# Optimization experiments

Hardware: AMD Instinct MI355X
Metric: run time of the kernel (lower is better)

The kernel has to match this reference:

```python
import jax, jax.numpy as jnp
import numpy as np

B, S, H = 128, 4096, 128

def setup_inputs() -> dict:
    key = jax.random.key(0)
    ks = jax.random.split(key, 6)
    return {
        "nodes_hidden": jax.random.normal(ks[0], (B, S, H), dtype=jnp.float32),
        "new_nodes": jax.random.normal(ks[1], (B, 1, H), dtype=jnp.float32),
        "W1": jax.random.normal(ks[2], (2 * H, 256), dtype=jnp.float32) * 0.06,
        "b1": jnp.zeros((256,), dtype=jnp.float32),
        "W2": jax.random.normal(ks[3], (256, 64), dtype=jnp.float32) * 0.06,
        "b2": jnp.zeros((64,), dtype=jnp.float32),
        "W3": jax.random.normal(ks[4], (64, 1), dtype=jnp.float32) * 0.1,
        "b3": jnp.zeros((1,), dtype=jnp.float32),
    }

def reference(nodes_hidden, new_nodes, W1, b1, W2, b2, W3, b3):
    # new_nodes: [B,1,H] -> broadcast over S; concat on feature axis -> [B,S,2H]
    new = jnp.broadcast_to(new_nodes, nodes_hidden.shape)
    con = jnp.concatenate([nodes_hidden, new], axis=-1)  # [B,S,2H]
    # MLP (dropout inactive at inference): 2H -> 256 -> 64 -> 1, batched over B*S
    h1 = jax.nn.relu(jnp.einsum('bsf,fk->bsk', con, W1) + b1)
    h2 = jax.nn.relu(jnp.einsum('bsk,km->bsm', h1, W2) + b2)
    out = jax.nn.sigmoid(jnp.einsum('bsm,mo->bso', h2, W3) + b3)  # [B,S,1]
    return jnp.squeeze(out, axis=-1)  # [B,S]
```

## Files before the change

kernel.cpp:

```cpp
#include <hip/hip_runtime.h>
#include <hip/hip_bf16.h>
#include <cstdint>
#include <cstddef>

#define BB 128
#define SS 4096
#define HH 128
#define N1 256
#define N2 64
#define BROWS 128

typedef __bf16 bf16x8 __attribute__((ext_vector_type(8)));
typedef __bf16 bf16x4 __attribute__((ext_vector_type(4)));
typedef float  f32x4  __attribute__((ext_vector_type(4)));

__global__ __launch_bounds__(256) void conv_weights(
    const float* __restrict__ W1, const float* __restrict__ W2,
    __bf16* __restrict__ w1f, __bf16* __restrict__ w2f)
{
    int tid = blockIdx.x * 256 + threadIdx.x;
    if (tid < 4096) {
        int lane = tid & 63, ks = (tid >> 6) & 3, g = tid >> 8;
        int col = 16 * g + (lane & 15);
        int kbase = 32 * ks + 8 * (lane >> 4);
        bf16x8 v;
#pragma unroll
        for (int j = 0; j < 8; ++j) v[j] = (__bf16)W1[(size_t)(kbase + j) * N1 + col];
        *(bf16x8*)(w1f + (size_t)tid * 8) = v;
    } else if (tid < 6144) {
        int s = tid - 4096;
        int lane = s & 63, ksp = (s >> 6) & 7, mt2 = s >> 9;
        int q = lane >> 4, ln = lane & 15;
        bf16x8 v;
#pragma unroll
        for (int j = 0; j < 8; ++j) {
            int c = 32 * ksp + 16 * (j >> 2) + 4 * q + (j & 3);
            v[j] = (__bf16)W2[(size_t)c * N2 + 16 * mt2 + ln];
        }
        *(bf16x8*)(w2f + (size_t)s * 8) = v;
    }
}

__global__ __launch_bounds__(256) void an_partial(
    const float* __restrict__ W1, const float* __restrict__ b1,
    const float* __restrict__ newn, __bf16* __restrict__ an)
{
    const int b = blockIdx.x, c = threadIdx.x;
    float acc = b1[c];
    const float* wp = W1 + (size_t)HH * N1 + c;
    const float* nv = newn + (size_t)b * HH;
#pragma unroll 8
    for (int k = 0; k < HH; ++k)
        acc = fmaf(nv[k], wp[(size_t)k * N1], acc);
    an[(size_t)b * N1 + c] = (__bf16)acc;
}

__global__ __launch_bounds__(256, 4) void edge_mlp_mfma4(
    const float* __restrict__ nodes,
    const float* __restrict__ b2,
    const float* __restrict__ W3, const float* __restrict__ b3,
    const __bf16* __restrict__ w1f, const __bf16* __restrict__ w2f,
    const __bf16* __restrict__ an,
    float* __restrict__ out)
{
    __shared__ __bf16 X[BROWS * HH];

    const int t = threadIdx.x;
    const int w = t >> 6, l = t & 63, q = l >> 4, ln = l & 15;
    const size_t row0 = (size_t)blockIdx.x * BROWS;
    const int b = (int)(row0 >> 12);

#pragma unroll
    for (int i = 0; i < 8; ++i) {
        int idx = i * 256 + t;
        int r = idx >> 4, c8 = idx & 15;
        const float* s = nodes + (row0 + r) * HH + 8 * c8;
        float4 f0 = *(const float4*)s, f1 = *(const float4*)(s + 4);
        bf16x8 v;
        v[0] = (__bf16)f0.x; v[1] = (__bf16)f0.y; v[2] = (__bf16)f0.z; v[3] = (__bf16)f0.w;
        v[4] = (__bf16)f1.x; v[5] = (__bf16)f1.y; v[6] = (__bf16)f1.z; v[7] = (__bf16)f1.w;
        int unit = c8 ^ (r & 7);
        *(bf16x8*)&X[(size_t)(r * 16 + unit) * 8] = v;
    }
    __syncthreads();

    f32x4 acc2[2][4];
#pragma unroll
    for (int mt2 = 0; mt2 < 4; ++mt2) {
        float4 bv = *(const float4*)(b2 + 16 * mt2 + 4 * q);
#pragma unroll
        for (int rs = 0; rs < 2; ++rs) {
            acc2[rs][mt2][0] = bv.x; acc2[rs][mt2][1] = bv.y;
            acc2[rs][mt2][2] = bv.z; acc2[rs][mt2][3] = bv.w;
        }
    }

    const __bf16* anb = an + (size_t)b * N1;

#pragma unroll 1
    for (int ksp = 0; ksp < 8; ++ksp) {
        bf16x8 af0[4], af1[4], a2f[4];
#pragma unroll
        for (int ks = 0; ks < 4; ++ks) {
            af0[ks] = *(const bf16x8*)(w1f + ((size_t)((2 * ksp)     * 4 + ks) * 64 + l) * 8);
            af1[ks] = *(const bf16x8*)(w1f + ((size_t)((2 * ksp + 1) * 4 + ks) * 64 + l) * 8);
        }
#pragma unroll
        for (int mt2 = 0; mt2 < 4; ++mt2)
            a2f[mt2] = *(const bf16x8*)(w2f + ((size_t)(mt2 * 8 + ksp) * 64 + l) * 8);

        f32x4 an0, an1;
        {
            bf16x4 a0 = *(const bf16x4*)(anb + 32 * ksp + 4 * q);
            bf16x4 a1 = *(const bf16x4*)(anb + 32 * ksp + 16 + 4 * q);
#pragma unroll
            for (int j = 0; j < 4; ++j) { an0[j] = (float)a0[j]; an1[j] = (float)a1[j]; }
        }

#pragma unroll
        for (int rs = 0; rs < 2; ++rs) {
            const int r = 32 * w + 16 * rs + ln;
            const int rx = ln & 7;
            f32x4 alo = an0, ahi = an1;
#pragma unroll
            for (int ks = 0; ks < 4; ++ks) {
                bf16x8 xv = *(const bf16x8*)&X[(size_t)(r * 16 + ((4 * ks + q) ^ rx)) * 8];
                alo = __builtin_amdgcn_mfma_f32_16x16x32_bf16(af0[ks], xv, alo, 0, 0, 0);
                ahi = __builtin_amdgcn_mfma_f32_16x16x32_bf16(af1[ks], xv, ahi, 0, 0, 0);
            }
            bf16x8 bfrag;
#pragma unroll
            for (int j = 0; j < 4; ++j) {
                bfrag[j]     = (__bf16)fmaxf(alo[j], 0.0f);
                bfrag[4 + j] = (__bf16)fmaxf(ahi[j], 0.0f);
            }
#pragma unroll
            for (int mt2 = 0; mt2 < 4; ++mt2)
                acc2[rs][mt2] = __builtin_amdgcn_mfma_f32_16x16x32_bf16(a2f[mt2], bfrag, acc2[rs][mt2], 0, 0, 0);
        }
    }

    const float b3v = b3[0];
#pragma unroll
    for (int rs = 0; rs < 2; ++rs) {
        float sum = 0.f;
#pragma unroll
        for (int mt2 = 0; mt2 < 4; ++mt2) {
            float4 w3v = *(const float4*)(W3 + 16 * mt2 + 4 * q);
            sum += fmaxf(acc2[rs][mt2][0], 0.f) * w3v.x
                 + fmaxf(acc2[rs][mt2][1], 0.f) * w3v.y
                 + fmaxf(acc2[rs][mt2][2], 0.f) * w3v.z
                 + fmaxf(acc2[rs][mt2][3], 0.f) * w3v.w;
        }
        sum += __shfl_xor(sum, 16, 64);
        sum += __shfl_xor(sum, 32, 64);
        if (q == 0) {
            float v = sum + b3v;
            out[row0 + 32 * w + 16 * rs + ln] = 1.0f / (1.0f + __expf(-v));
        }
    }
}

__global__ __launch_bounds__(256, 4) void edge_mlp_f32(
    const float* __restrict__ nodes, const float* __restrict__ newn,
    const float* __restrict__ W1, const float* __restrict__ b1,
    const float* __restrict__ W2, const float* __restrict__ b2,
    const float* __restrict__ W3, const float* __restrict__ b3,
    float* __restrict__ out)
{
    __shared__ float buf[32][256];
    const int t = threadIdx.x;
    const long r0 = (long)blockIdx.x * 32;
    const int b = (int)(r0 >> 12);
    const float4* src = (const float4*)(nodes + (size_t)r0 * HH);
#pragma unroll
    for (int i = 0; i < 4; ++i) {
        int idx = t + i * 256;
        *(float4*)&buf[idx >> 5][(idx & 31) * 4] = src[idx];
    }
    {
        float nv = newn[b * HH + (t & 127)];
        for (int r = (t >> 7); r < 32; r += 2) buf[r][HH + (t & 127)] = nv;
    }
    __syncthreads();
    const int c0 = t & 63, rb = (t >> 6) * 8;
    float acc[8][4];
#pragma unroll
    for (int ci = 0; ci < 4; ++ci) {
        float bv = b1[c0 + 64 * ci];
#pragma unroll
        for (int r = 0; r < 8; ++r) acc[r][ci] = bv;
    }
    for (int k = 0; k < 256; k += 4) {
        float wv[4][4];
#pragma unroll
        for (int kk = 0; kk < 4; ++kk)
#pragma unroll
            for (int ci = 0; ci < 4; ++ci) wv[kk][ci] = W1[(k + kk) * N1 + c0 + 64 * ci];
#pragma unroll
        for (int r = 0; r < 8; ++r) {
            float4 x = *(const float4*)&buf[rb + r][k];
#pragma unroll
            for (int ci = 0; ci < 4; ++ci) {
                acc[r][ci] = fmaf(x.x, wv[0][ci], acc[r][ci]);
                acc[r][ci] = fmaf(x.y, wv[1][ci], acc[r][ci]);
                acc[r][ci] = fmaf(x.z, wv[2][ci], acc[r][ci]);
                acc[r][ci] = fmaf(x.w, wv[3][ci], acc[r][ci]);
            }
        }
    }
    __syncthreads();
#pragma unroll
    for (int r = 0; r < 8; ++r)
#pragma unroll
        for (int ci = 0; ci < 4; ++ci) buf[rb + r][c0 + 64 * ci] = fmaxf(acc[r][ci], 0.0f);
    __syncthreads();
    const int c2 = t & 31, g2 = t >> 5;
    float acc2[4][2];
#pragma unroll
    for (int cj = 0; cj < 2; ++cj) {
        float bv = b2[c2 + 32 * cj];
#pragma unroll
        for (int rr = 0; rr < 4; ++rr) acc2[rr][cj] = bv;
    }
    for (int k = 0; k < 256; k += 4) {
        float w2v[4][2];
#pragma unroll
        for (int kk = 0; kk < 4; ++kk)
#pragma unroll
            for (int cj = 0; cj < 2; ++cj) w2v[kk][cj] = W2[(k + kk) * N2 + c2 + 32 * cj];
#pragma unroll
        for (int rr = 0; rr < 4; ++rr) {
            float4 x = *(const float4*)&buf[4 * g2 + rr][k];
#pragma unroll
            for (int cj = 0; cj < 2; ++cj) {
                acc2[rr][cj] = fmaf(x.x, w2v[0][cj], acc2[rr][cj]);
                acc2[rr][cj] = fmaf(x.y, w2v[1][cj], acc2[rr][cj]);
                acc2[rr][cj] = fmaf(x.z, w2v[2][cj], acc2[rr][cj]);
                acc2[rr][cj] = fmaf(x.w, w2v[3][cj], acc2[rr][cj]);
            }
        }
    }
    const float w3a = W3[c2], w3b = W3[c2 + 32], b3v = b3[0];
    float p[4];
#pragma unroll
    for (int rr = 0; rr < 4; ++rr)
        p[rr] = fmaf(fmaxf(acc2[rr][0], 0.f), w3a, fmaxf(acc2[rr][1], 0.f) * w3b);
#pragma unroll
    for (int off = 16; off >= 1; off >>= 1)
#pragma unroll
        for (int rr = 0; rr < 4; ++rr) p[rr] += __shfl_xor(p[rr], off, 64);
    if (c2 == 0)
#pragma unroll
        for (int rr = 0; rr < 4; ++rr)
            out[r0 + 4 * g2 + rr] = 1.0f / (1.0f + __expf(-(p[rr] + b3v)));
}

extern "C" void kernel_launch(void* const* d_in, const int* in_sizes, int n_in,
                              void* d_out, int out_size, void* d_ws, size_t ws_size,
                              hipStream_t stream) {
    const float* nodes = (const float*)d_in[0];
    const float* newn  = (const float*)d_in[1];
    const float* W1    = (const float*)d_in[2];
    const float* b1    = (const float*)d_in[3];
    const float* W2    = (const float*)d_in[4];
    const float* b2    = (const float*)d_in[5];
    const float* W3    = (const float*)d_in[6];
    const float* b3    = (const float*)d_in[7];
    float* out = (float*)d_out;
    const int M = BB * SS;

    if (ws_size >= 163840) {
        __bf16* w1f = (__bf16*)d_ws;
        __bf16* w2f = (__bf16*)d_ws + 32768;
        __bf16* anp = (__bf16*)d_ws + 49152;
        hipLaunchKernelGGL(conv_weights, dim3(24), dim3(256), 0, stream, W1, W2, w1f, w2f);
        hipLaunchKernelGGL(an_partial, dim3(BB), dim3(256), 0, stream, W1, b1, newn, anp);
        hipLaunchKernelGGL(edge_mlp_mfma4, dim3(M / BROWS), dim3(256), 0, stream,
                           nodes, b2, W3, b3, w1f, w2f, anp, out);
    } else {
        hipLaunchKernelGGL(edge_mlp_f32, dim3(M / 32), dim3(256), 0, stream,
                           nodes, newn, W1, b1, W2, b2, W3, b3, out);
    }
}
```

Baseline: 97.76 us.

## Load node rows directly into MFMA fragments, drop LDS staging, double rows per block

Result: no change. 96.74 us (-1.0%).

```diff
diff --git a/kernel.cpp b/kernel.cpp
--- a/kernel.cpp
+++ b/kernel.cpp
@@ -8,7 +8,7 @@
 #define HH 128
 #define N1 256
 #define N2 64
-#define BROWS 128
+#define BROWS 256
 
 typedef __bf16 bf16x8 __attribute__((ext_vector_type(8)));
 typedef __bf16 bf16x4 __attribute__((ext_vector_type(4)));
@@ -55,7 +55,7 @@
     an[(size_t)b * N1 + c] = (__bf16)acc;
 }
 
-__global__ __launch_bounds__(256, 4) void edge_mlp_mfma4(
+__global__ __launch_bounds__(256, 2) void edge_mlp_mfma5(
     const float* __restrict__ nodes,
     const float* __restrict__ b2,
     const float* __restrict__ W3, const float* __restrict__ b3,
@@ -63,33 +63,32 @@
     const __bf16* __restrict__ an,
     float* __restrict__ out)
 {
-    __shared__ __bf16 X[BROWS * HH];
-
     const int t = threadIdx.x;
     const int w = t >> 6, l = t & 63, q = l >> 4, ln = l & 15;
     const size_t row0 = (size_t)blockIdx.x * BROWS;
     const int b = (int)(row0 >> 12);
 
-#pragma unroll
-    for (int i = 0; i < 8; ++i) {
-        int idx = i * 256 + t;
-        int r = idx >> 4, c8 = idx & 15;
-        const float* s = nodes + (row0 + r) * HH + 8 * c8;
-        float4 f0 = *(const float4*)s, f1 = *(const float4*)(s + 4);
-        bf16x8 v;
-        v[0] = (__bf16)f0.x; v[1] = (__bf16)f0.y; v[2] = (__bf16)f0.z; v[3] = (__bf16)f0.w;
-        v[4] = (__bf16)f1.x; v[5] = (__bf16)f1.y; v[6] = (__bf16)f1.z; v[7] = (__bf16)f1.w;
-        int unit = c8 ^ (r & 7);
-        *(bf16x8*)&X[(size_t)(r * 16 + unit) * 8] = v;
-    }
-    __syncthreads();
-
-    f32x4 acc2[2][4];
+    bf16x8 xf[4][4];
+#pragma unroll
+    for (int rs = 0; rs < 4; ++rs) {
+        const float* rp = nodes + (row0 + 64 * w + 16 * rs + ln) * HH + 8 * q;
+#pragma unroll
+        for (int ks = 0; ks < 4; ++ks) {
+            float4 f0 = *(const float4*)(rp + 32 * ks);
+            float4 f1 = *(const float4*)(rp + 32 * ks + 4);
+            bf16x8 v;
+            v[0] = (__bf16)f0.x; v[1] = (__bf16)f0.y; v[2] = (__bf16)f0.z; v[3] = (__bf16)f0.w;
+            v[4] = (__bf16)f1.x; v[5] = (__bf16)f1.y; v[6] = (__bf16)f1.z; v[7] = (__bf16)f1.w;
+            xf[rs][ks] = v;
+        }
+    }
+
+    f32x4 acc2[4][4];
 #pragma unroll
     for (int mt2 = 0; mt2 < 4; ++mt2) {
         float4 bv = *(const float4*)(b2 + 16 * mt2 + 4 * q);
 #pragma unroll
-        for (int rs = 0; rs < 2; ++rs) {
+        for (int rs = 0; rs < 4; ++rs) {
             acc2[rs][mt2][0] = bv.x; acc2[rs][mt2][1] = bv.y;
             acc2[rs][mt2][2] = bv.z; acc2[rs][mt2][3] = bv.w;
         }
@@ -118,15 +117,12 @@
         }
 
 #pragma unroll
-        for (int rs = 0; rs < 2; ++rs) {
-            const int r = 32 * w + 16 * rs + ln;
-            const int rx = ln & 7;
+        for (int rs = 0; rs < 4; ++rs) {
             f32x4 alo = an0, ahi = an1;
 #pragma unroll
             for (int ks = 0; ks < 4; ++ks) {
-                bf16x8 xv = *(const bf16x8*)&X[(size_t)(r * 16 + ((4 * ks + q) ^ rx)) * 8];
-                alo = __builtin_amdgcn_mfma_f32_16x16x32_bf16(af0[ks], xv, alo, 0, 0, 0);
-                ahi = __builtin_amdgcn_mfma_f32_16x16x32_bf16(af1[ks], xv, ahi, 0, 0, 0);
+                alo = __builtin_amdgcn_mfma_f32_16x16x32_bf16(af0[ks], xf[rs][ks], alo, 0, 0, 0);
+                ahi = __builtin_amdgcn_mfma_f32_16x16x32_bf16(af1[ks], xf[rs][ks], ahi, 0, 0, 0);
             }
             bf16x8 bfrag;
 #pragma unroll
@@ -141,22 +137,24 @@
     }
 
     const float b3v = b3[0];
-#pragma unroll
-    for (int rs = 0; rs < 2; ++rs) {
+    float4 w3v[4];
+#pragma unroll
+    for (int mt2 = 0; mt2 < 4; ++mt2) w3v[mt2] = *(const float4*)(W3 + 16 * mt2 + 4 * q);
+#pragma unroll
+    for (int rs = 0; rs < 4; ++rs) {
         float sum = 0.f;
 #pragma unroll
         for (int mt2 = 0; mt2 < 4; ++mt2) {
-            float4 w3v = *(const float4*)(W3 + 16 * mt2 + 4 * q);
-            sum += fmaxf(acc2[rs][mt2][0], 0.f) * w3v.x
-                 + fmaxf(acc2[rs][mt2][1], 0.f) * w3v.y
-                 + fmaxf(acc2[rs][mt2][2], 0.f) * w3v.z
-                 + fmaxf(acc2[rs][mt2][3], 0.f) * w3v.w;
+            sum += fmaxf(acc2[rs][mt2][0], 0.f) * w3v[mt2].x
+                 + fmaxf(acc2[rs][mt2][1], 0.f) * w3v[mt2].y
+                 + fmaxf(acc2[rs][mt2][2], 0.f) * w3v[mt2].z
+                 + fmaxf(acc2[rs][mt2][3], 0.f) * w3v[mt2].w;
         }
         sum += __shfl_xor(sum, 16, 64);
         sum += __shfl_xor(sum, 32, 64);
         if (q == 0) {
             float v = sum + b3v;
-            out[row0 + 32 * w + 16 * rs + ln] = 1.0f / (1.0f + __expf(-v));
+            out[row0 + 64 * w + 16 * rs + ln] = 1.0f / (1.0f + __expf(-v));
         }
     }
 }
@@ -276,7 +274,7 @@
         __bf16* anp = (__bf16*)d_ws + 49152;
         hipLaunchKernelGGL(conv_weights, dim3(24), dim3(256), 0, stream, W1, W2, w1f, w2f);
         hipLaunchKernelGGL(an_partial, dim3(BB), dim3(256), 0, stream, W1, b1, newn, anp);
-        hipLaunchKernelGGL(edge_mlp_mfma4, dim3(M / BROWS), dim3(256), 0, stream,
+        hipLaunchKernelGGL(edge_mlp_mfma5, dim3(M / BROWS), dim3(256), 0, stream,
                            nodes, b2, W3, b3, w1f, w2f, anp, out);
     } else {
         hipLaunchKernelGGL(edge_mlp_f32, dim3(M / 32), dim3(256), 0, stream,
```

## Stage MLP weights in LDS per 1024-thread block, load node rows into registers

Applied to the files above, without the earlier changes.

After: 93.13 us. 4.7% less time.

```diff
diff --git a/kernel.cpp b/kernel.cpp
--- a/kernel.cpp
+++ b/kernel.cpp
@@ -8,62 +8,61 @@
 #define HH 128
 #define N1 256
 #define N2 64
-#define BROWS 128
+#define BROWS 512
 
 typedef __bf16 bf16x8 __attribute__((ext_vector_type(8)));
 typedef __bf16 bf16x4 __attribute__((ext_vector_type(4)));
 typedef float  f32x4  __attribute__((ext_vector_type(4)));
 
-__global__ __launch_bounds__(256) void conv_weights(
+__global__ __launch_bounds__(256) void prologue(
     const float* __restrict__ W1, const float* __restrict__ W2,
-    __bf16* __restrict__ w1f, __bf16* __restrict__ w2f)
+    const float* __restrict__ b1, const float* __restrict__ newn,
+    __bf16* __restrict__ w1f, __bf16* __restrict__ w2f, __bf16* __restrict__ an)
 {
-    int tid = blockIdx.x * 256 + threadIdx.x;
-    if (tid < 4096) {
-        int lane = tid & 63, ks = (tid >> 6) & 3, g = tid >> 8;
-        int col = 16 * g + (lane & 15);
-        int kbase = 32 * ks + 8 * (lane >> 4);
-        bf16x8 v;
-#pragma unroll
-        for (int j = 0; j < 8; ++j) v[j] = (__bf16)W1[(size_t)(kbase + j) * N1 + col];
-        *(bf16x8*)(w1f + (size_t)tid * 8) = v;
-    } else if (tid < 6144) {
-        int s = tid - 4096;
-        int lane = s & 63, ksp = (s >> 6) & 7, mt2 = s >> 9;
-        int q = lane >> 4, ln = lane & 15;
-        bf16x8 v;
-#pragma unroll
-        for (int j = 0; j < 8; ++j) {
-            int c = 32 * ksp + 16 * (j >> 2) + 4 * q + (j & 3);
-            v[j] = (__bf16)W2[(size_t)c * N2 + 16 * mt2 + ln];
-        }
-        *(bf16x8*)(w2f + (size_t)s * 8) = v;
-    }
-}
-
-__global__ __launch_bounds__(256) void an_partial(
-    const float* __restrict__ W1, const float* __restrict__ b1,
-    const float* __restrict__ newn, __bf16* __restrict__ an)
-{
-    const int b = blockIdx.x, c = threadIdx.x;
-    float acc = b1[c];
-    const float* wp = W1 + (size_t)HH * N1 + c;
-    const float* nv = newn + (size_t)b * HH;
+    const int blk = blockIdx.x;
+    if (blk < 24) {
+        int tid = blk * 256 + threadIdx.x;
+        if (tid < 4096) {
+            int lane = tid & 63, ks = (tid >> 6) & 3, g = tid >> 8;
+            int col = 16 * g + (lane & 15);
+            int kbase = 32 * ks + 8 * (lane >> 4);
+            bf16x8 v;
+#pragma unroll
+            for (int j = 0; j < 8; ++j) v[j] = (__bf16)W1[(size_t)(kbase + j) * N1 + col];
+            *(bf16x8*)(w1f + (size_t)tid * 8) = v;
+        } else {
+            int s = tid - 4096;
+            int lane = s & 63, ksp = (s >> 6) & 7, mt2 = s >> 9;
+            int q = lane >> 4, ln = lane & 15;
+            bf16x8 v;
+#pragma unroll
+            for (int j = 0; j < 8; ++j) {
+                int c = 32 * ksp + 16 * (j >> 2) + 4 * q + (j & 3);
+                v[j] = (__bf16)W2[(size_t)c * N2 + 16 * mt2 + ln];
+            }
+            *(bf16x8*)(w2f + (size_t)s * 8) = v;
+        }
+    } else {
+        const int b = blk - 24, c = threadIdx.x;
+        float acc = b1[c];
+        const float* wp = W1 + (size_t)HH * N1 + c;
+        const float* nv = newn + (size_t)b * HH;
 #pragma unroll 8
-    for (int k = 0; k < HH; ++k)
-        acc = fmaf(nv[k], wp[(size_t)k * N1], acc);
-    an[(size_t)b * N1 + c] = (__bf16)acc;
-}
-
-__global__ __launch_bounds__(256, 4) void edge_mlp_mfma4(
+        for (int k = 0; k < HH; ++k)
+            acc = fmaf(nv[k], wp[(size_t)k * N1], acc);
+        an[(size_t)b * N1 + c] = (__bf16)acc;
+    }
+}
+
+__global__ __launch_bounds__(1024, 4) void edge_mlp_mfma6(
     const float* __restrict__ nodes,
     const float* __restrict__ b2,
     const float* __restrict__ W3, const float* __restrict__ b3,
-    const __bf16* __restrict__ w1f, const __bf16* __restrict__ w2f,
+    const __bf16* __restrict__ wsrc,
     const __bf16* __restrict__ an,
     float* __restrict__ out)
 {
-    __shared__ __bf16 X[BROWS * HH];
+    __shared__ __bf16 wsm[49152];
 
     const int t = threadIdx.x;
     const int w = t >> 6, l = t & 63, q = l >> 4, ln = l & 15;
@@ -71,18 +70,25 @@
     const int b = (int)(row0 >> 12);
 
 #pragma unroll
-    for (int i = 0; i < 8; ++i) {
-        int idx = i * 256 + t;
-        int r = idx >> 4, c8 = idx & 15;
-        const float* s = nodes + (row0 + r) * HH + 8 * c8;
-        float4 f0 = *(const float4*)s, f1 = *(const float4*)(s + 4);
-        bf16x8 v;
-        v[0] = (__bf16)f0.x; v[1] = (__bf16)f0.y; v[2] = (__bf16)f0.z; v[3] = (__bf16)f0.w;
-        v[4] = (__bf16)f1.x; v[5] = (__bf16)f1.y; v[6] = (__bf16)f1.z; v[7] = (__bf16)f1.w;
-        int unit = c8 ^ (r & 7);
-        *(bf16x8*)&X[(size_t)(r * 16 + unit) * 8] = v;
-    }
-    __syncthreads();
+    for (int i = 0; i < 6; ++i) {
+        int idx = i * 1024 + t;
+        ((uint4*)wsm)[idx] = ((const uint4*)wsrc)[idx];
+    }
+
+    bf16x8 xf[2][4];
+#pragma unroll
+    for (int rs = 0; rs < 2; ++rs) {
+        const float* rp = nodes + (row0 + 32 * w + 16 * rs + ln) * HH + 8 * q;
+#pragma unroll
+        for (int ks = 0; ks < 4; ++ks) {
+            float4 f0 = *(const float4*)(rp + 32 * ks);
+            float4 f1 = *(const float4*)(rp + 32 * ks + 4);
+            bf16x8 v;
+            v[0] = (__bf16)f0.x; v[1] = (__bf16)f0.y; v[2] = (__bf16)f0.z; v[3] = (__bf16)f0.w;
+            v[4] = (__bf16)f1.x; v[5] = (__bf16)f1.y; v[6] = (__bf16)f1.z; v[7] = (__bf16)f1.w;
+            xf[rs][ks] = v;
+        }
+    }
 
     f32x4 acc2[2][4];
 #pragma unroll
@@ -96,18 +102,22 @@
     }
 
     const __bf16* anb = an + (size_t)b * N1;
+    const __bf16* w1s = wsm;
+    const __bf16* w2s = wsm + 32768;
+
+    __syncthreads();
 
 #pragma unroll 1
     for (int ksp = 0; ksp < 8; ++ksp) {
         bf16x8 af0[4], af1[4], a2f[4];
 #pragma unroll
         for (int ks = 0; ks < 4; ++ks) {
-            af0[ks] = *(const bf16x8*)(w1f + ((size_t)((2 * ksp)     * 4 + ks) * 64 + l) * 8);
-            af1[ks] = *(const bf16x8*)(w1f + ((size_t)((2 * ksp + 1) * 4 + ks) * 64 + l) * 8);
+            af0[ks] = *(const bf16x8*)(w1s + ((size_t)((2 * ksp)     * 4 + ks) * 64 + l) * 8);
+            af1[ks] = *(const bf16x8*)(w1s + ((size_t)((2 * ksp + 1) * 4 + ks) * 64 + l) * 8);
         }
 #pragma unroll
         for (int mt2 = 0; mt2 < 4; ++mt2)
-            a2f[mt2] = *(const bf16x8*)(w2f + ((size_t)(mt2 * 8 + ksp) * 64 + l) * 8);
+            a2f[mt2] = *(const bf16x8*)(w2s + ((size_t)(mt2 * 8 + ksp) * 64 + l) * 8);
 
         f32x4 an0, an1;
         {
@@ -119,14 +129,11 @@
 
 #pragma unroll
         for (int rs = 0; rs < 2; ++rs) {
-            const int r = 32 * w + 16 * rs + ln;
-            const int rx = ln & 7;
             f32x4 alo = an0, ahi = an1;
 #pragma unroll
             for (int ks = 0; ks < 4; ++ks) {
-                bf16x8 xv = *(const bf16x8*)&X[(size_t)(r * 16 + ((4 * ks + q) ^ rx)) * 8];
-                alo = __builtin_amdgcn_mfma_f32_16x16x32_bf16(af0[ks], xv, alo, 0, 0, 0);
-                ahi = __builtin_amdgcn_mfma_f32_16x16x32_bf16(af1[ks], xv, ahi, 0, 0, 0);
+                alo = __builtin_amdgcn_mfma_f32_16x16x32_bf16(af0[ks], xf[rs][ks], alo, 0, 0, 0);
+                ahi = __builtin_amdgcn_mfma_f32_16x16x32_bf16(af1[ks], xf[rs][ks], ahi, 0, 0, 0);
             }
             bf16x8 bfrag;
 #pragma unroll
@@ -274,10 +281,10 @@
         __bf16* w1f = (__bf16*)d_ws;
         __bf16* w2f = (__bf16*)d_ws + 32768;
         __bf16* anp = (__bf16*)d_ws + 49152;
-        hipLaunchKernelGGL(conv_weights, dim3(24), dim3(256), 0, stream, W1, W2, w1f, w2f);
-        hipLaunchKernelGGL(an_partial, dim3(BB), dim3(256), 0, stream, W1, b1, newn, anp);
-        hipLaunchKernelGGL(edge_mlp_mfma4, dim3(M / BROWS), dim3(256), 0, stream,
-                           nodes, b2, W3, b3, w1f, w2f, anp, out);
+        hipLaunchKernelGGL(prologue, dim3(24 + BB), dim3(256), 0, stream,
+                           W1, W2, b1, newn, w1f, w2f, anp);
+        hipLaunchKernelGGL(edge_mlp_mfma6, dim3(M / BROWS), dim3(1024), 0, stream,
+                           nodes, b2, W3, b3, w1f, anp, out);
     } else {
         hipLaunchKernelGGL(edge_mlp_f32, dim3(M / 32), dim3(256), 0, stream,
                            nodes, newn, W1, b1, W2, b2, W3, b3, out);
```
